# Kernel optimization log

Measured on AMD Instinct MI355X. Metric: run time of the kernel, lower is better.

## Reference

```python
import jax, jax.numpy as jnp
import numpy as np

B, S, H = 2, 2048, 4096
NH, NKV, HD = 32, 8, 128
ROPE_THETA = 10000.0


def setup_inputs() -> dict:
    key = jax.random.key(0)
    ks = jax.random.split(key, 5)
    hidden_states = jax.random.normal(ks[0], (B, S, H), dtype=jnp.float32)
    position_ids = jnp.tile(jnp.arange(S, dtype=jnp.int64)[None, :], (B, 1))
    Wq = jax.random.normal(ks[1], (H, NH * HD), dtype=jnp.float32) * 0.02
    Wk = jax.random.normal(ks[2], (H, NKV * HD), dtype=jnp.float32) * 0.02
    Wv = jax.random.normal(ks[3], (H, NKV * HD), dtype=jnp.float32) * 0.02
    Wo = jax.random.normal(ks[4], (NH * HD, H), dtype=jnp.float32) * 0.02
    return {"hidden_states": hidden_states, "position_ids": position_ids,
            "Wq": Wq, "Wk": Wk, "Wv": Wv, "Wo": Wo}


def _rotate_half(x):
    d = x.shape[-1] // 2
    return jnp.concatenate([-x[..., d:], x[..., :d]], axis=-1)


def reference(hidden_states, position_ids, Wq, Wk, Wv, Wo):
    b, s, _ = hidden_states.shape
    # QKV projections (no bias)
    q = (hidden_states @ Wq).reshape(b, s, NH, HD).transpose(0, 2, 1, 3)   # [b,nh,s,hd]
    k = (hidden_states @ Wk).reshape(b, s, NKV, HD).transpose(0, 2, 1, 3)  # [b,nkv,s,hd]
    v = (hidden_states @ Wv).reshape(b, s, NKV, HD).transpose(0, 2, 1, 3)
    # RoPE: cos/sin from cached table == analytic computation at position_ids
    inv_freq = 1.0 / (ROPE_THETA ** (jnp.arange(0, HD, 2, dtype=jnp.float32) / HD))
    freqs = position_ids.astype(jnp.float32)[:, :, None] * inv_freq  # [b,s,hd/2]
    emb = jnp.concatenate([freqs, freqs], axis=-1)                   # [b,s,hd]
    cos = jnp.cos(emb)[:, None, :, :]  # unsqueeze_dim=1 -> [b,1,s,hd]
    sin = jnp.sin(emb)[:, None, :, :]
    q = q * cos + _rotate_half(q) * sin
    k = k * cos + _rotate_half(k) * sin
    # GQA: repeat kv heads to match query heads
    groups = NH // NKV
    k = jnp.repeat(k, groups, axis=1)
    v = jnp.repeat(v, groups, axis=1)
    # causal SDPA
    scale = 1.0 / jnp.sqrt(jnp.float32(HD))
    scores = jnp.einsum('bhqd,bhkd->bhqk', q, k) * scale
    causal = jnp.tril(jnp.ones((s, s), dtype=bool))
    scores = jnp.where(causal[None, None], scores, jnp.finfo(scores.dtype).min)
    attn = jax.nn.softmax(scores, axis=-1)
    out = jnp.einsum('bhqk,bhkd->bhqd', attn, v)
    out = out.transpose(0, 2, 1, 3).reshape(b, s, NH * HD)
    return out @ Wo
```

## Files before the change

### kernel.cpp

```cpp
#include <hip/hip_runtime.h>
#include <cstdint>
#include <cstddef>

typedef unsigned short u16;
typedef unsigned int u32;
typedef short short8 __attribute__((ext_vector_type(8)));
typedef float f32x4 __attribute__((ext_vector_type(4)));

__device__ __forceinline__ u16 f2bf(float f) {
  unsigned u = __float_as_uint(f);
  u += 0x7fffu + ((u >> 16) & 1u);
  return (u16)(u >> 16);
}
__device__ __forceinline__ float bf2f(u16 h) {
  return __uint_as_float(((unsigned)h) << 16);
}
__device__ __forceinline__ u32 pack_bf2(float lo, float hi) {
  return ((u32)f2bf(hi) << 16) | (u32)f2bf(lo);
}

typedef const __attribute__((address_space(1))) unsigned int gu32_t;
typedef __attribute__((address_space(3))) unsigned int su32_t;
__device__ __forceinline__ void gl2lds16(const void* g, void* l) {
  __builtin_amdgcn_global_load_lds((gu32_t*)g, (su32_t*)l, 16, 0, 0);
}

__device__ __forceinline__ f32x4 mfma_bf16(short8 a, short8 b, f32x4 c) {
  return __builtin_amdgcn_mfma_f32_16x16x32_bf16(a, b, c, 0, 0, 0);
}

__global__ __launch_bounds__(256) void f32_to_bf16_kernel(
    const float* __restrict__ x, u16* __restrict__ y, int n) {
  int i = (blockIdx.x * 256 + threadIdx.x) * 4;
  if (i + 3 < n) {
    float4 v = *(const float4*)(x + i);
    ushort4 o;
    o.x = f2bf(v.x); o.y = f2bf(v.y); o.z = f2bf(v.z); o.w = f2bf(v.w);
    *(ushort4*)(y + i) = o;
  }
}

__global__ __launch_bounds__(256) void transpose_w_kernel(
    const float* __restrict__ W, u16* __restrict__ Wt, int K, int N) {
  __shared__ float tile[32][33];
  int n0 = blockIdx.x * 32, k0 = blockIdx.y * 32;
  int tx = threadIdx.x, ty = threadIdx.y;
#pragma unroll
  for (int j = 0; j < 4; ++j)
    tile[ty + j * 8][tx] = W[(size_t)(k0 + ty + j * 8) * N + n0 + tx];
  __syncthreads();
#pragma unroll
  for (int j = 0; j < 4; ++j)
    Wt[(size_t)(n0 + ty + j * 8) * K + k0 + tx] = f2bf(tile[tx][ty + j * 8]);
}

__device__ __forceinline__ void tile_compute(const u16* __restrict__ as,
                                             const u16* __restrict__ bs,
                                             f32x4 (&acc)[8][4],
                                             int arow, int brow, int qoff) {
  short8 bfr[4], afr[4];
#pragma unroll
  for (int n = 0; n < 4; ++n)
    bfr[n] = *(const short8*)&bs[(brow + n * 16) * 32 + qoff];
#pragma unroll
  for (int m = 0; m < 4; ++m)
    afr[m] = *(const short8*)&as[(arow + m * 16) * 32 + qoff];
  __builtin_amdgcn_s_setprio(1);
#pragma unroll
  for (int m = 0; m < 4; ++m)
#pragma unroll
    for (int n = 0; n < 4; ++n)
      acc[m][n] = mfma_bf16(afr[m], bfr[n], acc[m][n]);
  __builtin_amdgcn_s_setprio(0);
#pragma unroll
  for (int m = 0; m < 4; ++m)
    afr[m] = *(const short8*)&as[(arow + (4 + m) * 16) * 32 + qoff];
  __builtin_amdgcn_s_setprio(1);
#pragma unroll
  for (int m = 0; m < 4; ++m)
#pragma unroll
    for (int n = 0; n < 4; ++n)
      acc[4 + m][n] = mfma_bf16(afr[m], bfr[n], acc[4 + m][n]);
  __builtin_amdgcn_s_setprio(0);
}

#define STAGE256(slot_, ko_)                                     \
  do {                                                           \
    u16* as_ = &lds4[slot_][0][0];                               \
    u16* bs_ = &lds4[slot_][1][0];                               \
    gl2lds16(ap + (ko_), as_ + w * 512);                         \
    gl2lds16(ap + (size_t)128 * K + (ko_), as_ + 4096 + w * 512);\
    gl2lds16(bp + (ko_), bs_ + w * 512);                         \
    gl2lds16(bp + (size_t)128 * K + (ko_), bs_ + 4096 + w * 512);\
  } while (0)

#define SBAR()                          \
  do {                                  \
    asm volatile("" ::: "memory");      \
    __builtin_amdgcn_s_barrier();       \
    asm volatile("" ::: "memory");      \
  } while (0)

template <bool BF16OUT>
__global__ __launch_bounds__(512, 2) void gemm_bt_256(
    const u16* __restrict__ A, const u16* __restrict__ Bt,
    float* __restrict__ Cf, u16* __restrict__ Cb, int K, int ldc) {
  __shared__ alignas(16) u16 lds4[4][2][8192];
  const int tid = threadIdx.x;
  const int w = tid >> 6, lane = tid & 63;
  const int lq = lane & 15, qd = lane >> 4;
  const int wm = w >> 2, wn = w & 3;
  const int m0 = blockIdx.y * 256, n0 = blockIdx.x * 256;
  const int r4 = lane >> 2;
  const int csw = ((lane & 3) ^ ((lane >> 3) & 3)) * 8;
  const int qoff = (qd ^ ((lq >> 1) & 3)) * 8;
  const int arow = wm * 128 + lq, brow = wn * 64 + lq;

  f32x4 acc[8][4] = {};
  const u16* ap = A + ((size_t)(m0 + w * 16 + r4) * K + csw);
  const u16* bp = Bt + ((size_t)(n0 + w * 16 + r4) * K + csw);
  const int nt = K >> 5;

  STAGE256(0, 0);
  STAGE256(1, 32);
  STAGE256(2, 64);

  for (int t = 0; t + 3 < nt; ++t) {
    STAGE256((t + 3) & 3, (t + 3) * 32);
    asm volatile("s_waitcnt vmcnt(12)" ::: "memory");
    SBAR();
    tile_compute(&lds4[t & 3][0][0], &lds4[t & 3][1][0], acc, arow, brow, qoff);
    SBAR();
  }
  asm volatile("s_waitcnt vmcnt(8)" ::: "memory");
  SBAR();
  tile_compute(&lds4[(nt - 3) & 3][0][0], &lds4[(nt - 3) & 3][1][0], acc, arow, brow, qoff);
  asm volatile("s_waitcnt vmcnt(4)" ::: "memory");
  SBAR();
  tile_compute(&lds4[(nt - 2) & 3][0][0], &lds4[(nt - 2) & 3][1][0], acc, arow, brow, qoff);
  asm volatile("s_waitcnt vmcnt(0)" ::: "memory");
  SBAR();
  tile_compute(&lds4[(nt - 1) & 3][0][0], &lds4[(nt - 1) & 3][1][0], acc, arow, brow, qoff);

#pragma unroll
  for (int m = 0; m < 8; ++m) {
    const int row = m0 + wm * 128 + m * 16 + qd * 4;
#pragma unroll
    for (int n = 0; n < 4; ++n) {
      const int col = n0 + wn * 64 + n * 16 + lq;
#pragma unroll
      for (int r = 0; r < 4; ++r) {
        if (BF16OUT)
          Cb[(size_t)(row + r) * ldc + col] = f2bf(acc[m][n][r]);
        else
          Cf[(size_t)(row + r) * ldc + col] = acc[m][n][r];
      }
    }
  }
}

#undef STAGE256

__global__ __launch_bounds__(256) void rope_kernel(
    const u16* __restrict__ src, u16* __restrict__ dst,
    const int* __restrict__ pos_ids, int nh, int src_col0, int dst_ld, int total,
    float scale) {
  int idx = blockIdx.x * 256 + threadIdx.x;
  if (idx >= total) return;
  int i = idx & 63;
  int t = idx >> 6;
  int hh = t % nh;
  int m = t / nh;
  float pos = (float)pos_ids[m];
  float inv = exp2f(-(float)i * 0.20762050593046016f);
  float f = pos * inv;
  float c = cosf(f) * scale, s = sinf(f) * scale;
  const u16* sp = src + (size_t)m * 6144 + src_col0 + hh * 128;
  float x0 = bf2f(sp[i]);
  float x1 = bf2f(sp[i + 64]);
  u16* dp = dst + (size_t)m * dst_ld + hh * 128;
  dp[i] = f2bf(x0 * c - x1 * s);
  dp[i + 64] = f2bf(x1 * c + x0 * s);
}

__global__ __launch_bounds__(256) void vt_kernel(
    const u16* __restrict__ src, u16* __restrict__ vt) {
  __shared__ u16 tile[32][33];
  int s0 = blockIdx.x * 32;
  int d0 = blockIdx.y * 32;
  int bz = blockIdx.z;
  int b = bz >> 3, kvh = bz & 7;
  int tx = threadIdx.x, ty = threadIdx.y;
#pragma unroll
  for (int j = 0; j < 4; ++j)
    tile[ty + j * 8][tx] =
        src[(size_t)(b * 2048 + s0 + ty + j * 8) * 6144 + 5120 + kvh * 128 + d0 + tx];
  __syncthreads();
#pragma unroll
  for (int j = 0; j < 4; ++j)
    vt[((size_t)(b * 8 + kvh) * 128 + d0 + ty + j * 8) * 2048 + s0 + tx] =
        tile[tx][ty + j * 8];
}

#define PS_LD 76
__global__ __launch_bounds__(256, 3) void flash_kernel(
    const u16* __restrict__ Q, const u16* __restrict__ K,
    const u16* __restrict__ Vt, u16* __restrict__ O) {
  __shared__ alignas(16) u16 Ks[64 * 128];
  __shared__ alignas(16) u16 Vs[128 * 64];
  __shared__ alignas(16) u16 Ps[4][32 * PS_LD];

  const int tid = threadIdx.x;
  const int w = tid >> 6, lane = tid & 63;
  const int lq = lane & 15, qd = lane >> 4;
  const int lq7 = lq & 7;
  const int bh = blockIdx.y;
  const int b = bh >> 5, h = bh & 31, kvh = h >> 2;
  const int q0 = (gridDim.x - 1 - blockIdx.x) * 128;

  short8 qf[2][4];
  {
    const u16* qp = Q + ((size_t)(b * 2048 + q0 + w * 32 + lq) * 4096 + h * 128 + qd * 8);
#pragma unroll
    for (int n = 0; n < 2; ++n)
#pragma unroll
      for (int ks = 0; ks < 4; ++ks)
        qf[n][ks] = *(const short8*)(qp + (size_t)n * 16 * 4096 + ks * 32);
  }

  f32x4 ot[2][8] = {};
  float mprev[2], lsum[2];
#pragma unroll
  for (int n = 0; n < 2; ++n) { mprev[n] = -1e30f; lsum[n] = 0.f; }

  const int rk = lane >> 4;
  const int pk = lane & 15;
  const int ckA = (pk ^ rk) * 8;
  const int ckB = (pk ^ (4 + rk)) * 8;
  const int rv = lane >> 3;
  const int cv = ((lane & 7) ^ rv) * 8;

  const int kv_end = q0 + 128;

  for (int kv0 = 0; kv0 < kv_end; kv0 += 64) {
    {
      const u16* kbase = K + ((size_t)(b * 2048 + kv0 + w * 16 + rk) * 1024) + kvh * 128;
#pragma unroll
      for (int i = 0; i < 4; ++i)
        gl2lds16(kbase + (size_t)(i * 4) * 1024 + ((i & 1) ? ckB : ckA),
                 &Ks[(w * 16 + i * 4) * 128]);
      const u16* vbase = Vt + ((size_t)((b * 8 + kvh) * 128 + w * 32 + rv) * 2048) + kv0 + cv;
#pragma unroll
      for (int i = 0; i < 4; ++i)
        gl2lds16(vbase + (size_t)(i * 8) * 2048, &Vs[(w * 32 + i * 8) * 64]);
    }
    __syncthreads();

    f32x4 st[4][2] = {};
#pragma unroll
    for (int ks = 0; ks < 4; ++ks) {
      short8 kf[4];
#pragma unroll
      for (int m = 0; m < 4; ++m)
        kf[m] = *(const short8*)&Ks[(m * 16 + lq) * 128 + ((ks * 4 + qd) ^ lq7) * 8];
#pragma unroll
      for (int m = 0; m < 4; ++m)
#pragma unroll
        for (int n = 0; n < 2; ++n)
          st[m][n] = mfma_bf16(kf[m], qf[n][ks], st[m][n]);
    }

    if (kv0 + 63 > q0) {
#pragma unroll
      for (int n = 0; n < 2; ++n) {
        const int qrow = q0 + w * 32 + n * 16 + lq;
#pragma unroll
        for (int m = 0; m < 4; ++m) {
          const int kvb = kv0 + m * 16 + qd * 4;
#pragma unroll
          for (int r = 0; r < 4; ++r)
            if (kvb + r > qrow) st[m][n][r] = -1e30f;
        }
      }
    }

#pragma unroll
    for (int n = 0; n < 2; ++n) {
      float t = st[0][n][0];
#pragma unroll
      for (int m = 0; m < 4; ++m)
#pragma unroll
        for (int r = 0; r < 4; ++r) t = fmaxf(t, st[m][n][r]);
      t = fmaxf(t, __shfl_xor(t, 16));
      t = fmaxf(t, __shfl_xor(t, 32));
      const float mnew = fmaxf(mprev[n], t);
      const float alpha = __expf(mprev[n] - mnew);
      mprev[n] = mnew;

      float rs = 0.f;
      u32 pk2[4][2];
#pragma unroll
      for (int m = 0; m < 4; ++m) {
        float p0 = __expf(st[m][n][0] - mnew);
        float p1 = __expf(st[m][n][1] - mnew);
        float p2 = __expf(st[m][n][2] - mnew);
        float p3 = __expf(st[m][n][3] - mnew);
        rs += (p0 + p1) + (p2 + p3);
        pk2[m][0] = pack_bf2(p0, p1);
        pk2[m][1] = pack_bf2(p2, p3);
      }
      rs += __shfl_xor(rs, 16);
      rs += __shfl_xor(rs, 32);
      lsum[n] = lsum[n] * alpha + rs;

      u16* pw = &Ps[w][(n * 16 + lq) * PS_LD + qd * 4];
#pragma unroll
      for (int m = 0; m < 4; ++m)
        *(uint2*)(pw + m * 16) = make_uint2(pk2[m][0], pk2[m][1]);

#pragma unroll
      for (int mt = 0; mt < 8; ++mt)
#pragma unroll
        for (int r = 0; r < 4; ++r) ot[n][mt][r] *= alpha;
    }

#pragma unroll
    for (int kst = 0; kst < 2; ++kst) {
      short8 bp[2];
#pragma unroll
      for (int n = 0; n < 2; ++n)
        bp[n] = *(const short8*)&Ps[w][(n * 16 + lq) * PS_LD + kst * 32 + qd * 8];
#pragma unroll
      for (int mt = 0; mt < 8; ++mt) {
        short8 av = *(const short8*)&Vs[(mt * 16 + lq) * 64 + ((kst * 4 + qd) ^ lq7) * 8];
#pragma unroll
        for (int n = 0; n < 2; ++n)
          ot[n][mt] = mfma_bf16(av, bp[n], ot[n][mt]);
      }
    }
    __syncthreads();
  }

#pragma unroll
  for (int n = 0; n < 2; ++n) {
    const float inv = 1.f / lsum[n];
    const size_t row = (size_t)(b * 2048 + q0 + w * 32 + n * 16 + lq);
    u16* op = O + row * 4096 + h * 128 + qd * 4;
#pragma unroll
    for (int mt = 0; mt < 8; ++mt) {
      u32 a = pack_bf2(ot[n][mt][0] * inv, ot[n][mt][1] * inv);
      u32 c = pack_bf2(ot[n][mt][2] * inv, ot[n][mt][3] * inv);
      *(uint2*)(op + mt * 16) = make_uint2(a, c);
    }
  }
}

extern "C" void kernel_launch(void* const* d_in, const int* in_sizes, int n_in,
                              void* d_out, int out_size, void* d_ws, size_t ws_size,
                              hipStream_t stream) {
  const float* hidden = (const float*)d_in[0];
  const int* pos = (const int*)d_in[1];
  const float* Wq = (const float*)d_in[2];
  const float* Wk = (const float*)d_in[3];
  const float* Wv = (const float*)d_in[4];
  const float* Wo = (const float*)d_in[5];
  float* out = (float*)d_out;

  char* ws = (char*)d_ws;
  u16* hbf   = (u16*)(ws);
  u16* wqkvt = (u16*)(ws + 33554432ull);
  u16* wot   = (u16*)(ws + 83886080ull);
  u16* qkvbf = (u16*)(ws + 117440512ull);
  u16* qbf   = (u16*)(ws + 167772160ull);
  u16* kbf   = (u16*)(ws + 201326592ull);
  u16* vt    = (u16*)(ws + 209715200ull);
  u16* obf   = (u16*)(ws + 218103808ull);

  f32_to_bf16_kernel<<<16384, 256, 0, stream>>>(hidden, hbf, 16777216);
  transpose_w_kernel<<<dim3(128, 128), dim3(32, 8), 0, stream>>>(Wq, wqkvt, 4096, 4096);
  transpose_w_kernel<<<dim3(32, 128), dim3(32, 8), 0, stream>>>(Wk, wqkvt + (size_t)4096 * 4096, 4096, 1024);
  transpose_w_kernel<<<dim3(32, 128), dim3(32, 8), 0, stream>>>(Wv, wqkvt + (size_t)5120 * 4096, 4096, 1024);
  transpose_w_kernel<<<dim3(128, 128), dim3(32, 8), 0, stream>>>(Wo, wot, 4096, 4096);

  gemm_bt_256<true><<<dim3(24, 16), 512, 0, stream>>>(hbf, wqkvt, nullptr, qkvbf, 4096, 6144);

  rope_kernel<<<32768, 256, 0, stream>>>(qkvbf, qbf, pos, 32, 0, 4096, 8388608, 0.08838834764831845f);
  rope_kernel<<<8192, 256, 0, stream>>>(qkvbf, kbf, pos, 8, 4096, 1024, 2097152, 1.0f);

  vt_kernel<<<dim3(64, 4, 16), dim3(32, 8), 0, stream>>>(qkvbf, vt);

  flash_kernel<<<dim3(16, 64), 256, 0, stream>>>(qbf, kbf, vt, obf);

  gemm_bt_256<false><<<dim3(16, 16), 512, 0, stream>>>(obf, wot, out, nullptr, 4096, 4096);
}
```

Before: 907.2 us.

## Pair causal query tiles per block and register-prefetch next K/V tile

Each flash block now processes two query tiles, a long one (15-p) and a short one (p), so every block does the same amount of causal work. The grid is halved to 8x64 blocks. K/V loading moves from direct global-to-LDS loads to register prefetch of the next tile during compute, followed by an LDS store between barriers. MFMA sections are raised in priority with s_setprio. Occupancy drops from 3 to 2 blocks per CU, and the register pressure from prefetch buffers could cost some latency hiding.

```diff
diff --git a/kernel.cpp b/kernel.cpp
--- a/kernel.cpp
+++ b/kernel.cpp
@@ -203,7 +203,35 @@
 }
 
 #define PS_LD 76
-__global__ __launch_bounds__(256, 3) void flash_kernel(
+
+__device__ __forceinline__ void load_q_frag(short8 (&qf)[2][4], const u16* __restrict__ Q,
+                                            int b, int q0, int w, int lq, int qd, int h) {
+  const u16* qp = Q + ((size_t)(b * 2048 + q0 + w * 32 + lq) * 4096 + h * 128 + qd * 8);
+#pragma unroll
+  for (int n = 0; n < 2; ++n)
+#pragma unroll
+    for (int ks = 0; ks < 4; ++ks)
+      qf[n][ks] = *(const short8*)(qp + (size_t)n * 16 * 4096 + ks * 32);
+}
+
+__device__ __forceinline__ void store_o(u16* __restrict__ O, const f32x4 (&ot)[2][8],
+                                        const float* lsum, int b, int q0,
+                                        int w, int lq, int qd, int h) {
+#pragma unroll
+  for (int n = 0; n < 2; ++n) {
+    const float inv = 1.f / lsum[n];
+    const size_t row = (size_t)(b * 2048 + q0 + w * 32 + n * 16 + lq);
+    u16* op = O + row * 4096 + h * 128 + qd * 4;
+#pragma unroll
+    for (int mt = 0; mt < 8; ++mt) {
+      u32 a = pack_bf2(ot[n][mt][0] * inv, ot[n][mt][1] * inv);
+      u32 c = pack_bf2(ot[n][mt][2] * inv, ot[n][mt][3] * inv);
+      *(uint2*)(op + mt * 16) = make_uint2(a, c);
+    }
+  }
+}
+
+__global__ __launch_bounds__(256, 2) void flash_kernel(
     const u16* __restrict__ Q, const u16* __restrict__ K,
     const u16* __restrict__ Vt, u16* __restrict__ O) {
   __shared__ alignas(16) u16 Ks[64 * 128];
@@ -216,45 +244,65 @@
   const int lq7 = lq & 7;
   const int bh = blockIdx.y;
   const int b = bh >> 5, h = bh & 31, kvh = h >> 2;
-  const int q0 = (gridDim.x - 1 - blockIdx.x) * 128;
-
-  short8 qf[2][4];
-  {
-    const u16* qp = Q + ((size_t)(b * 2048 + q0 + w * 32 + lq) * 4096 + h * 128 + qd * 8);
-#pragma unroll
-    for (int n = 0; n < 2; ++n)
-#pragma unroll
-      for (int ks = 0; ks < 4; ++ks)
-        qf[n][ks] = *(const short8*)(qp + (size_t)n * 16 * 4096 + ks * 32);
-  }
-
-  f32x4 ot[2][8] = {};
-  float mprev[2], lsum[2];
-#pragma unroll
-  for (int n = 0; n < 2; ++n) { mprev[n] = -1e30f; lsum[n] = 0.f; }
-
-  const int rk = lane >> 4;
-  const int pk = lane & 15;
-  const int ckA = (pk ^ rk) * 8;
-  const int ckB = (pk ^ (4 + rk)) * 8;
+  const int p = blockIdx.x;
+  const int nhi = 32 - 2 * p;
+  const int nlo = 2 * p + 2;
+  const int nsteps = nhi + nlo;
+
+  const int rk = lane >> 4, pk = lane & 15;
+  const int ckA = (pk ^ rk) * 8, ckB = (pk ^ (4 + rk)) * 8;
   const int rv = lane >> 3;
   const int cv = ((lane & 7) ^ rv) * 8;
 
-  const int kv_end = q0 + 128;
-
-  for (int kv0 = 0; kv0 < kv_end; kv0 += 64) {
-    {
-      const u16* kbase = K + ((size_t)(b * 2048 + kv0 + w * 16 + rk) * 1024) + kvh * 128;
-#pragma unroll
-      for (int i = 0; i < 4; ++i)
-        gl2lds16(kbase + (size_t)(i * 4) * 1024 + ((i & 1) ? ckB : ckA),
-                 &Ks[(w * 16 + i * 4) * 128]);
-      const u16* vbase = Vt + ((size_t)((b * 8 + kvh) * 128 + w * 32 + rv) * 2048) + kv0 + cv;
-#pragma unroll
-      for (int i = 0; i < 4; ++i)
-        gl2lds16(vbase + (size_t)(i * 8) * 2048, &Vs[(w * 32 + i * 8) * 64]);
-    }
-    __syncthreads();
+  const u16* ksrc = K + ((size_t)(b * 2048 + w * 16 + rk) * 1024) + kvh * 128;
+  const u16* vsrc = Vt + ((size_t)((b * 8 + kvh) * 128 + w * 32 + rv) * 2048) + cv;
+  u16* kdst = &Ks[(w * 16) * 128] + lane * 8;
+  u16* vdst = &Vs[(w * 32) * 64] + lane * 8;
+
+  int q0 = (15 - p) * 128;
+  short8 qf[2][4];
+  load_q_frag(qf, Q, b, q0, w, lq, qd, h);
+
+  f32x4 ot[2][8] = {};
+  float mprev[2] = {-1e30f, -1e30f}, lsum[2] = {0.f, 0.f};
+
+  uint4 kreg[4], vreg[4];
+  kreg[0] = *(const uint4*)(ksrc + ckA);
+  kreg[1] = *(const uint4*)(ksrc + 4096 + ckB);
+  kreg[2] = *(const uint4*)(ksrc + 8192 + ckA);
+  kreg[3] = *(const uint4*)(ksrc + 12288 + ckB);
+  vreg[0] = *(const uint4*)(vsrc);
+  vreg[1] = *(const uint4*)(vsrc + 8 * 2048);
+  vreg[2] = *(const uint4*)(vsrc + 16 * 2048);
+  vreg[3] = *(const uint4*)(vsrc + 24 * 2048);
+  *(uint4*)(kdst) = kreg[0];
+  *(uint4*)(kdst + 512) = kreg[1];
+  *(uint4*)(kdst + 1024) = kreg[2];
+  *(uint4*)(kdst + 1536) = kreg[3];
+  *(uint4*)(vdst) = vreg[0];
+  *(uint4*)(vdst + 512) = vreg[1];
+  *(uint4*)(vdst + 1024) = vreg[2];
+  *(uint4*)(vdst + 1536) = vreg[3];
+  asm volatile("s_waitcnt lgkmcnt(0)" ::: "memory");
+  __builtin_amdgcn_s_barrier();
+
+  for (int s = 0; s < nsteps; ++s) {
+    const int kv0 = (s < nhi ? s : s - nhi) * 64;
+
+    if (s + 1 < nsteps) {
+      const int sn = s + 1;
+      const int kv0n = (sn < nhi ? sn : sn - nhi) * 64;
+      const u16* kp_ = ksrc + (size_t)kv0n * 1024;
+      kreg[0] = *(const uint4*)(kp_ + ckA);
+      kreg[1] = *(const uint4*)(kp_ + 4096 + ckB);
+      kreg[2] = *(const uint4*)(kp_ + 8192 + ckA);
+      kreg[3] = *(const uint4*)(kp_ + 12288 + ckB);
+      const u16* vp_ = vsrc + kv0n;
+      vreg[0] = *(const uint4*)(vp_);
+      vreg[1] = *(const uint4*)(vp_ + 8 * 2048);
+      vreg[2] = *(const uint4*)(vp_ + 16 * 2048);
+      vreg[3] = *(const uint4*)(vp_ + 24 * 2048);
+    }
 
     f32x4 st[4][2] = {};
 #pragma unroll
@@ -263,11 +311,13 @@
 #pragma unroll
       for (int m = 0; m < 4; ++m)
         kf[m] = *(const short8*)&Ks[(m * 16 + lq) * 128 + ((ks * 4 + qd) ^ lq7) * 8];
+      __builtin_amdgcn_s_setprio(1);
 #pragma unroll
       for (int m = 0; m < 4; ++m)
 #pragma unroll
         for (int n = 0; n < 2; ++n)
           st[m][n] = mfma_bf16(kf[m], qf[n][ks], st[m][n]);
+      __builtin_amdgcn_s_setprio(0);
     }
 
     if (kv0 + 63 > q0) {
@@ -333,26 +383,47 @@
 #pragma unroll
       for (int mt = 0; mt < 8; ++mt) {
         short8 av = *(const short8*)&Vs[(mt * 16 + lq) * 64 + ((kst * 4 + qd) ^ lq7) * 8];
+        __builtin_amdgcn_s_setprio(1);
 #pragma unroll
         for (int n = 0; n < 2; ++n)
           ot[n][mt] = mfma_bf16(av, bp[n], ot[n][mt]);
+        __builtin_amdgcn_s_setprio(0);
       }
     }
-    __syncthreads();
+
+    asm volatile("s_waitcnt lgkmcnt(0)" ::: "memory");
+    __builtin_amdgcn_s_barrier();
+
+    if (s + 1 < nsteps) {
+      *(uint4*)(kdst) = kreg[0];
+      *(uint4*)(kdst + 512) = kreg[1];
+      *(uint4*)(kdst + 1024) = kreg[2];
+      *(uint4*)(kdst + 1536) = kreg[3];
+      *(uint4*)(vdst) = vreg[0];
+      *(uint4*)(vdst + 512) = vreg[1];
+      *(uint4*)(vdst + 1024) = vreg[2];
+      *(uint4*)(vdst + 1536) = vreg[3];
+      asm volatile("s_waitcnt lgkmcnt(0)" ::: "memory");
+      __builtin_amdgcn_s_barrier();
+    }
+
+    if (s == nhi - 1) {
+      store_o(O, ot, lsum, b, q0, w, lq, qd, h);
+      q0 = p * 128;
+      load_q_frag(qf, Q, b, q0, w, lq, qd, h);
+#pragma unroll
+      for (int n = 0; n < 2; ++n) {
+        mprev[n] = -1e30f;
+        lsum[n] = 0.f;
+#pragma unroll
+        for (int mt = 0; mt < 8; ++mt)
+#pragma unroll
+          for (int r = 0; r < 4; ++r) ot[n][mt][r] = 0.f;
+      }
+    }
   }
 
-#pragma unroll
-  for (int n = 0; n < 2; ++n) {
-    const float inv = 1.f / lsum[n];
-    const size_t row = (size_t)(b * 2048 + q0 + w * 32 + n * 16 + lq);
-    u16* op = O + row * 4096 + h * 128 + qd * 4;
-#pragma unroll
-    for (int mt = 0; mt < 8; ++mt) {
-      u32 a = pack_bf2(ot[n][mt][0] * inv, ot[n][mt][1] * inv);
-      u32 c = pack_bf2(ot[n][mt][2] * inv, ot[n][mt][3] * inv);
-      *(uint2*)(op + mt * 16) = make_uint2(a, c);
-    }
-  }
+  store_o(O, ot, lsum, b, q0, w, lq, qd, h);
 }
 
 extern "C" void kernel_launch(void* const* d_in, const int* in_sizes, int n_in,
@@ -389,7 +460,7 @@
 
   vt_kernel<<<dim3(64, 4, 16), dim3(32, 8), 0, stream>>>(qkvbf, vt);
 
-  flash_kernel<<<dim3(16, 64), 256, 0, stream>>>(qbf, kbf, vt, obf);
+  flash_kernel<<<dim3(8, 64), 256, 0, stream>>>(qbf, kbf, vt, obf);
 
   gemm_bt_256<false><<<dim3(16, 16), 512, 0, stream>>>(obf, wot, out, nullptr, 4096, 4096);
 }
```

Result: faster. 868.5 us (-4.3%).
